# Kernel tuning notes

Measured on AMD Instinct MI355X. Metric: run time of the kernel, lower is better.

## Reference

```python
import jax, jax.numpy as jnp
import numpy as np

B, C, D = 2048, 8, 2048  # batch, channels, in_size == out_size
EPS = 1e-12


def setup_inputs() -> dict:
    key = jax.random.key(0)
    k1, k2, k3 = jax.random.split(key, 3)
    x = jax.random.normal(k1, (B, C, D), dtype=jnp.float32)
    # xavier_uniform over the last two dims (fan_in = fan_out = D)
    lim = float(np.sqrt(6.0 / (D + D)))
    Wq = jax.random.uniform(k2, (C, D, D), jnp.float32, -lim, lim)
    Wk = jax.random.uniform(k3, (C, D, D), jnp.float32, -lim, lim)
    Wq0 = jnp.zeros((C, D), jnp.float32)
    Wk0 = jnp.zeros((C, D), jnp.float32)
    return {"x": x, "Wq": Wq, "Wq0": Wq0, "Wk": Wk, "Wk0": Wk0}


def reference(x, Wq, Wq0, Wk, Wk0):
    # Per-channel projections: K[b,c,o] = sum_d x[b,c,d] * Wk[c,d,o] + Wk0[c,o]
    K = jnp.einsum('bcd,cdo->bco', x, Wk) + Wk0          # [B, C, D]
    Q = jnp.einsum('bcd,cdo->bco', x, Wq) + Wq0          # [B, C, D]
    # Unnormalized scores: Yu[o,c,p] = sum_b Q[b,c,o] * K[b,c,p]
    Yu = jnp.einsum('bco,bcp->ocp', Q, K)                # [D, C, D]
    # Batch-axis L2 norms squared: [D, C]
    DQ2 = jnp.sum(Q * Q, axis=0).T                       # DQ2[o,c]
    DK2 = jnp.sum(K * K, axis=0).T                       # DK2[p,c]
    # DQK[o,c,p] = sqrt(DQ2[o,c] * DK2[p,c]), clamped at eps
    DQK = jnp.maximum(jnp.sqrt(DQ2[:, :, None] * DK2.T[None, :, :]), EPS)
    Y = Yu / DQK                                         # cosine similarity scores
    SM = jax.nn.softmax(Y, axis=0)                       # softmax over first feature axis
    # Z[b,c,o] = sum_p x[b,c,p] * SM[p,c,o]
    Z = jnp.einsum('bcp,pco->bco', x, SM)                # [B, C, D]
    return Z
```

## Files before the change

kernel.cpp:

```cpp
#include <hip/hip_runtime.h>
#include <hip/hip_bf16.h>
#include <cstdint>
#include <cstddef>

#define NN 2048
#define CCH 8

using f32x4  = __attribute__((ext_vector_type(4))) float;
using bf16x8 = __attribute__((ext_vector_type(8))) __bf16;

__device__ __forceinline__ unsigned short f2bf(float f) {
  union { __bf16 b; unsigned short u; } v; v.b = (__bf16)f; return v.u;
}

__device__ __forceinline__ void async_load16(const void* gp, void* lp) {
  __builtin_amdgcn_global_load_lds(
      (__attribute__((address_space(1))) void*)(void*)gp,
      (__attribute__((address_space(3))) void*)lp, 16, 0, 0);
}

__global__ __launch_bounds__(256) void cast_x(const float* __restrict__ x,
                                              unsigned short* __restrict__ xb) {
  const size_t i4 = ((size_t)blockIdx.x * 256 + threadIdx.x) * 4;
  const int    d  = (int)(i4 & (NN - 1));
  const size_t t  = i4 >> 11;
  const int    ch = (int)(t & (CCH - 1));
  const size_t b  = t >> 3;
  const float4 v  = *(const float4*)(x + i4);
  ushort4 o;
  o.x = f2bf(v.x); o.y = f2bf(v.y); o.z = f2bf(v.z); o.w = f2bf(v.w);
  *(ushort4*)&xb[((size_t)ch * NN + b) * NN + d] = o;
}

__global__ __launch_bounds__(256) void transpose_cast(const float* __restrict__ Wq,
                                                      const float* __restrict__ Wk,
                                                      unsigned short* __restrict__ Wqt,
                                                      unsigned short* __restrict__ Wkt) {
  const int z  = blockIdx.z;
  const int ch = z & 7;
  const float* src          = (z < 8 ? Wq : Wk) + (size_t)ch * NN * NN;
  unsigned short* dst       = (z < 8 ? Wqt : Wkt) + (size_t)ch * NN * NN;
  __shared__ float tile[32][33];
  const int o0 = blockIdx.x * 32;
  const int d0 = blockIdx.y * 32;
  const int tx = threadIdx.x, ty = threadIdx.y;
#pragma unroll
  for (int k = 0; k < 4; ++k)
    tile[ty + 8 * k][tx] = src[(size_t)(d0 + ty + 8 * k) * NN + (o0 + tx)];
  __syncthreads();
#pragma unroll
  for (int k = 0; k < 4; ++k)
    dst[(size_t)(o0 + ty + 8 * k) * NN + (d0 + tx)] = f2bf(tile[tx][ty + 8 * k]);
}

template <int MODE>
__global__ __launch_bounds__(512, 2) void gemm_tn(const unsigned short* __restrict__ A,
                                                  const unsigned short* __restrict__ B,
                                                  void* __restrict__ Cout,
                                                  const float* __restrict__ rowP,
                                                  const float* __restrict__ colP,
                                                  float* __restrict__ accP) {
  const int    c  = blockIdx.z;
  const size_t MS = (size_t)NN * NN;
  const unsigned short* Ac = A + (size_t)c * MS;
  const unsigned short* Bc = B + (size_t)c * MS;

  __shared__ union __attribute__((aligned(16))) {
    struct { unsigned short As[2][256 * 64]; unsigned short Bs[2][256 * 64]; } t;
    float rsum[256];
  } sm;

  const int tid  = threadIdx.x;
  const int wave = tid >> 6;
  const int lane = tid & 63;
  const int wm   = wave >> 2;
  const int wn   = wave & 3;
  const int fr   = lane & 15;
  const int quad = lane >> 4;

  const int mBase = blockIdx.y * 256;
  const int nBase = blockIdx.x * 256;

  const int r0  = (wave << 3) + (lane >> 3);
  const int csw = (lane & 7) ^ (r0 & 7);
  const unsigned short* gA = Ac + (size_t)(mBase + r0) * NN + csw * 8;
  const unsigned short* gB = Bc + (size_t)(nBase + r0) * NN + csw * 8;

  f32x4  acc[8][4] = {};
  bf16x8 af[4][2];
  bf16x8 bf0[2][2];
  bf16x8 bf1[2][2];

#define STAGE_A(buf, h, kt)                                                              \
  {                                                                                      \
    const unsigned short* _s = gA + (size_t)((h) * 128) * NN + (size_t)(kt) * 64;        \
    async_load16(_s,                   &sm.t.As[buf][((h) * 128 +      wave * 8) * 64]); \
    async_load16(_s + (size_t)64 * NN, &sm.t.As[buf][((h) * 128 + 64 + wave * 8) * 64]); \
  }
#define STAGE_B(buf, h, kt)                                                              \
  {                                                                                      \
    const unsigned short* _s = gB + (size_t)((h) * 128) * NN + (size_t)(kt) * 64;        \
    async_load16(_s,                   &sm.t.Bs[buf][((h) * 128 +      wave * 8) * 64]); \
    async_load16(_s + (size_t)64 * NN, &sm.t.Bs[buf][((h) * 128 + 64 + wave * 8) * 64]); \
  }
#define LDA_(buf, h)                                                                      \
  _Pragma("unroll") for (int i = 0; i < 4; ++i)                                           \
  _Pragma("unroll") for (int kk = 0; kk < 2; ++kk)                                        \
    af[i][kk] = *(const bf16x8*)&sm.t.As[buf][(wm * 128 + (h) * 64 + i * 16 + fr) * 64 +  \
                                             (((kk << 2) | quad) ^ (fr & 7)) * 8];
#define LDB_(buf, g, arr)                                                                 \
  _Pragma("unroll") for (int j = 0; j < 2; ++j)                                           \
  _Pragma("unroll") for (int kk = 0; kk < 2; ++kk)                                        \
    arr[j][kk] = *(const bf16x8*)&sm.t.Bs[buf][(wn * 64 + (g) * 32 + j * 16 + fr) * 64 +  \
                                              (((kk << 2) | quad) ^ (fr & 7)) * 8];
#define MM_(h, g, arr)                                                                    \
  __builtin_amdgcn_s_setprio(1);                                                          \
  _Pragma("unroll") for (int i = 0; i < 4; ++i)                                           \
  _Pragma("unroll") for (int j = 0; j < 2; ++j) {                                         \
    acc[(h) * 4 + i][(g) * 2 + j] = __builtin_amdgcn_mfma_f32_16x16x32_bf16(              \
        af[i][0], arr[j][0], acc[(h) * 4 + i][(g) * 2 + j], 0, 0, 0);                     \
    acc[(h) * 4 + i][(g) * 2 + j] = __builtin_amdgcn_mfma_f32_16x16x32_bf16(              \
        af[i][1], arr[j][1], acc[(h) * 4 + i][(g) * 2 + j], 0, 0, 0);                     \
  }                                                                                       \
  __builtin_amdgcn_s_setprio(0);
#define FENCE_ asm volatile("" ::: "memory")
#define BAR_   { FENCE_; __builtin_amdgcn_s_barrier(); FENCE_; }
#define VM2_   asm volatile("s_waitcnt vmcnt(2)" ::: "memory")
#define VM0_   asm volatile("s_waitcnt vmcnt(0)" ::: "memory")

  STAGE_A(0, 0, 0); STAGE_A(0, 1, 0); STAGE_B(0, 0, 0); STAGE_B(0, 1, 0);
  STAGE_A(1, 0, 1);
  VM2_; BAR_;

#pragma unroll 1
  for (int it = 0; it < 15; ++it) {
    const int ko = 2 * it + 1;
    const int ke = 2 * it + 2;
    LDA_(0, 0); LDB_(0, 0, bf0); STAGE_A(1, 1, ko);
    BAR_; MM_(0, 0, bf0); BAR_;
    LDB_(0, 1, bf1); STAGE_B(1, 0, ko);
    BAR_; MM_(0, 1, bf1); BAR_;
    LDA_(0, 1); STAGE_B(1, 1, ko);
    BAR_; MM_(1, 0, bf0); BAR_;
    STAGE_A(0, 0, ke);
    BAR_; MM_(1, 1, bf1); VM2_; BAR_;
    LDA_(1, 0); LDB_(1, 0, bf0); STAGE_A(0, 1, ke);
    BAR_; MM_(0, 0, bf0); BAR_;
    LDB_(1, 1, bf1); STAGE_B(0, 0, ke);
    BAR_; MM_(0, 1, bf1); BAR_;
    LDA_(1, 1); STAGE_B(0, 1, ke);
    BAR_; MM_(1, 0, bf0); BAR_;
    STAGE_A(1, 0, ko + 2);
    BAR_; MM_(1, 1, bf1); VM2_; BAR_;
  }
  LDA_(0, 0); LDB_(0, 0, bf0); STAGE_A(1, 1, 31);
  BAR_; MM_(0, 0, bf0); BAR_;
  LDB_(0, 1, bf1); STAGE_B(1, 0, 31);
  BAR_; MM_(0, 1, bf1); BAR_;
  LDA_(0, 1); STAGE_B(1, 1, 31);
  BAR_; MM_(1, 0, bf0); BAR_;
  BAR_; MM_(1, 1, bf1); VM0_; BAR_;
  LDA_(1, 0); LDB_(1, 0, bf0);
  BAR_; MM_(0, 0, bf0); BAR_;
  LDB_(1, 1, bf1);
  BAR_; MM_(0, 1, bf1); BAR_;
  LDA_(1, 1);
  BAR_; MM_(1, 0, bf0); BAR_;
  MM_(1, 1, bf1);

  FENCE_;
  __syncthreads();

  if constexpr (MODE == 0) {
    if (tid < 256) sm.rsum[tid] = 0.0f;
    __syncthreads();
    unsigned short* Co = (unsigned short*)Cout + (size_t)c * MS;
    const float* biasC = rowP + c * NN;
    float* dsq         = accP + c * NN;
#pragma unroll
    for (int i = 0; i < 8; ++i) {
#pragma unroll
      for (int r = 0; r < 4; ++r) {
        const int lrow   = wm * 128 + i * 16 + quad * 4 + r;
        const int row    = mBase + lrow;
        const float bias = biasC[row];
        float ss = 0.0f;
#pragma unroll
        for (int j = 0; j < 4; ++j) {
          const int col = nBase + wn * 64 + j * 16 + fr;
          float v = acc[i][j][r] + bias;
          Co[(size_t)row * NN + col] = f2bf(v);
          ss += v * v;
        }
#pragma unroll
        for (int m = 8; m >= 1; m >>= 1) ss += __shfl_xor(ss, m, 64);
        if (fr == 0) atomicAdd(&sm.rsum[lrow], ss);
      }
    }
    __syncthreads();
    if (tid < 256) atomicAdd(&dsq[mBase + tid], sm.rsum[tid]);
  } else if constexpr (MODE == 1) {
    if (tid < 256) sm.rsum[tid] = 0.0f;
    __syncthreads();
    unsigned short* Co = (unsigned short*)Cout + (size_t)c * MS;
    const float* dk2C  = rowP + c * NN;
    const float* dq2C  = colP + c * NN;
    float* csum        = accP + c * NN;
    float dq[4];
#pragma unroll
    for (int j = 0; j < 4; ++j) dq[j] = dq2C[nBase + wn * 64 + j * 16 + fr];
#pragma unroll
    for (int i = 0; i < 8; ++i) {
#pragma unroll
      for (int r = 0; r < 4; ++r) {
        const int lrow = wm * 128 + i * 16 + quad * 4 + r;
        const int row  = mBase + lrow;
        const float dk = dk2C[row];
        float es = 0.0f;
#pragma unroll
        for (int j = 0; j < 4; ++j) {
          const int col = nBase + wn * 64 + j * 16 + fr;
          const float denom = fmaxf(sqrtf(dk * dq[j]), 1e-12f);
          const float e = __expf(acc[i][j][r] / denom);
          Co[(size_t)row * NN + col] = f2bf(e);
          es += e;
        }
#pragma unroll
        for (int m = 8; m >= 1; m >>= 1) es += __shfl_xor(es, m, 64);
        if (fr == 0) atomicAdd(&sm.rsum[lrow], es);
      }
    }
    __syncthreads();
    if (tid < 256) atomicAdd(&csum[mBase + tid], sm.rsum[tid]);
  } else {
    float* Co        = (float*)Cout;
    const float* csC = colP + c * NN;
    float rcs[4];
#pragma unroll
    for (int j = 0; j < 4; ++j) rcs[j] = 1.0f / csC[nBase + wn * 64 + j * 16 + fr];
#pragma unroll
    for (int i = 0; i < 8; ++i)
#pragma unroll
      for (int r = 0; r < 4; ++r) {
        const int row = mBase + wm * 128 + i * 16 + quad * 4 + r;
#pragma unroll
        for (int j = 0; j < 4; ++j) {
          const int col = nBase + wn * 64 + j * 16 + fr;
          Co[((size_t)row * CCH + c) * NN + col] = acc[i][j][r] * rcs[j];
        }
      }
  }
#undef STAGE_A
#undef STAGE_B
#undef LDA_
#undef LDB_
#undef MM_
#undef FENCE_
#undef BAR_
#undef VM2_
#undef VM0_
}

extern "C" void kernel_launch(void* const* d_in, const int* in_sizes, int n_in,
                              void* d_out, int out_size, void* d_ws, size_t ws_size,
                              hipStream_t stream) {
  const float* x   = (const float*)d_in[0];
  const float* Wq  = (const float*)d_in[1];
  const float* Wq0 = (const float*)d_in[2];
  const float* Wk  = (const float*)d_in[3];
  const float* Wk0 = (const float*)d_in[4];

  const size_t S = (size_t)NN * NN * CCH;
  char* ws = (char*)d_ws;
  unsigned short* xb  = (unsigned short*)(ws);
  unsigned short* Wqt = (unsigned short*)(ws + 2 * S);
  unsigned short* Wkt = (unsigned short*)(ws + 4 * S);
  unsigned short* Qt  = (unsigned short*)(ws + 6 * S);
  unsigned short* Kt  = (unsigned short*)(ws + 8 * S);
  unsigned short* Et  = Wqt;
  float* stats = (float*)(ws + 10 * S);
  float* dq2   = stats;
  float* dk2   = stats + CCH * NN;
  float* csum  = stats + 2 * CCH * NN;

  hipMemsetAsync(stats, 0, 3 * CCH * NN * sizeof(float), stream);
  cast_x<<<32768, 256, 0, stream>>>(x, xb);
  transpose_cast<<<dim3(64, 64, 16), dim3(32, 8), 0, stream>>>(Wq, Wk, Wqt, Wkt);

  dim3 gg(8, 8, 8);
  gemm_tn<0><<<gg, 512, 0, stream>>>(Wqt, xb, Qt, Wq0, nullptr, dq2);
  gemm_tn<0><<<gg, 512, 0, stream>>>(Wkt, xb, Kt, Wk0, nullptr, dk2);
  gemm_tn<1><<<gg, 512, 0, stream>>>(Kt, Qt, Et, dk2, dq2, csum);
  gemm_tn<2><<<gg, 512, 0, stream>>>(xb, Et, d_out, nullptr, csum, nullptr);
}
```

Before: 935.7 us.

## Vectorize weight transpose, remap GEMM blocks per XCD, front-load B staging

The weight transpose-cast kernel now uses 64x64 tiles with float4 loads and ushort4 stores instead of scalar accesses, cutting memory instructions. The GEMM grid is flattened to 1D and remapped so consecutive block IDs that round-robin across XCDs land on the same channel, aiming for better L2 locality. The pipeline also issues B-tile async loads earlier, pairing them with A loads in the same phase, to give them more latency slack. The risks are LDS bank conflicts in the wider transpose tile and uneven vmcnt accounting, since VM2 waits now see a different number of loads in flight.

```diff
diff --git a/kernel.cpp b/kernel.cpp
--- a/kernel.cpp
+++ b/kernel.cpp
@@ -38,19 +38,33 @@
                                                       unsigned short* __restrict__ Wkt) {
   const int z  = blockIdx.z;
   const int ch = z & 7;
-  const float* src          = (z < 8 ? Wq : Wk) + (size_t)ch * NN * NN;
-  unsigned short* dst       = (z < 8 ? Wqt : Wkt) + (size_t)ch * NN * NN;
-  __shared__ float tile[32][33];
-  const int o0 = blockIdx.x * 32;
-  const int d0 = blockIdx.y * 32;
-  const int tx = threadIdx.x, ty = threadIdx.y;
-#pragma unroll
-  for (int k = 0; k < 4; ++k)
-    tile[ty + 8 * k][tx] = src[(size_t)(d0 + ty + 8 * k) * NN + (o0 + tx)];
+  const float* src    = (z < 8 ? Wq : Wk) + (size_t)ch * NN * NN;
+  unsigned short* dst = (z < 8 ? Wqt : Wkt) + (size_t)ch * NN * NN;
+  __shared__ float tile[64][65];
+  const int o0 = blockIdx.x * 64;
+  const int d0 = blockIdx.y * 64;
+  const int t  = threadIdx.x;
+  const int tx = t & 15, ty = t >> 4;
+#pragma unroll
+  for (int k = 0; k < 4; ++k) {
+    const float4 v = *(const float4*)&src[(size_t)(d0 + ty + 16 * k) * NN + (o0 + tx * 4)];
+    tile[ty + 16 * k][tx * 4 + 0] = v.x;
+    tile[ty + 16 * k][tx * 4 + 1] = v.y;
+    tile[ty + 16 * k][tx * 4 + 2] = v.z;
+    tile[ty + 16 * k][tx * 4 + 3] = v.w;
+  }
   __syncthreads();
-#pragma unroll
-  for (int k = 0; k < 4; ++k)
-    dst[(size_t)(o0 + ty + 8 * k) * NN + (d0 + tx)] = f2bf(tile[tx][ty + 8 * k]);
+  const int ud = t & 15, uo = t >> 4;
+#pragma unroll
+  for (int k = 0; k < 4; ++k) {
+    const int o = uo + 16 * k;
+    ushort4 w;
+    w.x = f2bf(tile[ud * 4 + 0][o]);
+    w.y = f2bf(tile[ud * 4 + 1][o]);
+    w.z = f2bf(tile[ud * 4 + 2][o]);
+    w.w = f2bf(tile[ud * 4 + 3][o]);
+    *(ushort4*)&dst[(size_t)(o0 + o) * NN + d0 + ud * 4] = w;
+  }
 }
 
 template <int MODE>
@@ -60,7 +74,12 @@
                                                   const float* __restrict__ rowP,
                                                   const float* __restrict__ colP,
                                                   float* __restrict__ accP) {
-  const int    c  = blockIdx.z;
+  const int wg  = blockIdx.x;
+  const int lin = ((wg & 7) << 6) | (wg >> 3);
+  const int c   = lin >> 6;
+  const int by  = (lin >> 3) & 7;
+  const int bx  = lin & 7;
+
   const size_t MS = (size_t)NN * NN;
   const unsigned short* Ac = A + (size_t)c * MS;
   const unsigned short* Bc = B + (size_t)c * MS;
@@ -78,8 +97,8 @@
   const int fr   = lane & 15;
   const int quad = lane >> 4;
 
-  const int mBase = blockIdx.y * 256;
-  const int nBase = blockIdx.x * 256;
+  const int mBase = by * 256;
+  const int nBase = bx * 256;
 
   const int r0  = (wave << 3) + (lane >> 3);
   const int csw = (lane & 7) ^ (r0 & 7);
@@ -136,28 +155,28 @@
   for (int it = 0; it < 15; ++it) {
     const int ko = 2 * it + 1;
     const int ke = 2 * it + 2;
-    LDA_(0, 0); LDB_(0, 0, bf0); STAGE_A(1, 1, ko);
+    LDA_(0, 0); LDB_(0, 0, bf0); STAGE_A(1, 1, ko); STAGE_B(1, 0, ko);
     BAR_; MM_(0, 0, bf0); BAR_;
-    LDB_(0, 1, bf1); STAGE_B(1, 0, ko);
+    LDB_(0, 1, bf1); STAGE_B(1, 1, ko);
     BAR_; MM_(0, 1, bf1); BAR_;
-    LDA_(0, 1); STAGE_B(1, 1, ko);
+    LDA_(0, 1);
     BAR_; MM_(1, 0, bf0); BAR_;
     STAGE_A(0, 0, ke);
     BAR_; MM_(1, 1, bf1); VM2_; BAR_;
-    LDA_(1, 0); LDB_(1, 0, bf0); STAGE_A(0, 1, ke);
+    LDA_(1, 0); LDB_(1, 0, bf0); STAGE_A(0, 1, ke); STAGE_B(0, 0, ke);
     BAR_; MM_(0, 0, bf0); BAR_;
-    LDB_(1, 1, bf1); STAGE_B(0, 0, ke);
+    LDB_(1, 1, bf1); STAGE_B(0, 1, ke);
     BAR_; MM_(0, 1, bf1); BAR_;
-    LDA_(1, 1); STAGE_B(0, 1, ke);
+    LDA_(1, 1);
     BAR_; MM_(1, 0, bf0); BAR_;
     STAGE_A(1, 0, ko + 2);
     BAR_; MM_(1, 1, bf1); VM2_; BAR_;
   }
-  LDA_(0, 0); LDB_(0, 0, bf0); STAGE_A(1, 1, 31);
+  LDA_(0, 0); LDB_(0, 0, bf0); STAGE_A(1, 1, 31); STAGE_B(1, 0, 31);
   BAR_; MM_(0, 0, bf0); BAR_;
-  LDB_(0, 1, bf1); STAGE_B(1, 0, 31);
+  LDB_(0, 1, bf1); STAGE_B(1, 1, 31);
   BAR_; MM_(0, 1, bf1); BAR_;
-  LDA_(0, 1); STAGE_B(1, 1, 31);
+  LDA_(0, 1);
   BAR_; MM_(1, 0, bf0); BAR_;
   BAR_; MM_(1, 1, bf1); VM0_; BAR_;
   LDA_(1, 0); LDB_(1, 0, bf0);
@@ -285,11 +304,10 @@
 
   hipMemsetAsync(stats, 0, 3 * CCH * NN * sizeof(float), stream);
   cast_x<<<32768, 256, 0, stream>>>(x, xb);
-  transpose_cast<<<dim3(64, 64, 16), dim3(32, 8), 0, stream>>>(Wq, Wk, Wqt, Wkt);
-
-  dim3 gg(8, 8, 8);
-  gemm_tn<0><<<gg, 512, 0, stream>>>(Wqt, xb, Qt, Wq0, nullptr, dq2);
-  gemm_tn<0><<<gg, 512, 0, stream>>>(Wkt, xb, Kt, Wk0, nullptr, dk2);
-  gemm_tn<1><<<gg, 512, 0, stream>>>(Kt, Qt, Et, dk2, dq2, csum);
-  gemm_tn<2><<<gg, 512, 0, stream>>>(xb, Et, d_out, nullptr, csum, nullptr);
-}
+  transpose_cast<<<dim3(32, 32, 16), 256, 0, stream>>>(Wq, Wk, Wqt, Wkt);
+
+  gemm_tn<0><<<512, 512, 0, stream>>>(Wqt, xb, Qt, Wq0, nullptr, dq2);
+  gemm_tn<0><<<512, 512, 0, stream>>>(Wkt, xb, Kt, Wk0, nullptr, dk2);
+  gemm_tn<1><<<512, 512, 0, stream>>>(Kt, Qt, Et, dk2, dq2, csum);
+  gemm_tn<2><<<512, 512, 0, stream>>>(xb, Et, d_out, nullptr, csum, nullptr);
+}
```

After: 911.3 us. 1.03x faster.
